# Kernel optimization log

Hardware: AMD Instinct MI355X
Metric: run time of the kernel (lower is better)

## Reference

```python
import jax, jax.numpy as jnp
import numpy as np

BATCH, BANDS, RESOLUTION = 8, 128, 64
N_FRAMES, N_SAMPLES = 128, 32768


def setup_inputs() -> dict:
    key = jax.random.key(0)
    k1, k2, k3 = jax.random.split(key, 3)
    x = jax.random.normal(k1, (BATCH, BANDS, RESOLUTION), dtype=jnp.float32)
    gumbel_noise = jax.random.gumbel(k2, (BATCH, BANDS, RESOLUTION), dtype=jnp.float32)
    # stand-in for morlet filter bank buffer (1, bands, n_samples)
    filter_bank = jax.random.normal(k3, (1, BANDS, N_SAMPLES), dtype=jnp.float32)
    # resonance buffer: linspace(0, 0.999, resolution) repeated over frames, cumprod over frames
    res = jnp.broadcast_to(jnp.linspace(0.0, 0.999, RESOLUTION, dtype=jnp.float32)[:, None],
                           (RESOLUTION, N_FRAMES))
    resonance = jnp.cumprod(res, axis=-1)  # (resolution, n_frames)
    return {"x": x, "gumbel_noise": gumbel_noise, "filter_bank": filter_bank, "resonance": resonance}


def _linear_interp_last(r, n_samples):
    # PyTorch F.interpolate(mode='linear', align_corners=False) on last axis
    n_in = r.shape[-1]
    scale = n_in / n_samples
    pos = (jnp.arange(n_samples, dtype=jnp.float32) + 0.5) * scale - 0.5
    pos = jnp.clip(pos, 0.0, n_in - 1)
    lo = jnp.floor(pos).astype(jnp.int32)
    hi = jnp.minimum(lo + 1, n_in - 1)
    w = (pos - lo.astype(jnp.float32)).astype(r.dtype)
    return r[..., lo] * (1.0 - w) + r[..., hi] * w


def reference(x, gumbel_noise, filter_bank, resonance):
    # gumbel_softmax with tau=1, hard=False: softmax(logits + gumbel_noise)
    g = jax.nn.softmax(x + gumbel_noise, axis=-1)              # (b, bands, resolution)
    r = jnp.einsum('bcr,rf->bcf', g, resonance)                # (b, bands, n_frames)
    up = _linear_interp_last(r, filter_bank.shape[-1])         # (b, bands, n_samples)
    out = jnp.mean(up * filter_bank, axis=1, keepdims=True)    # (b, 1, n_samples)
    return out
```

## Files before the change

kernel.cpp:

```cpp
#include <hip/hip_runtime.h>
#include <hip/hip_bf16.h>


#define BATCH 8
#define BANDS 128
#define RES 64
#define NF 128
#define NS 32768
#define SEG 512
#define NSEG (NS / SEG)
#define NBP 4
#define NTHR 512

__global__ __launch_bounds__(NTHR) void fused(const float* __restrict__ x,
                                              const float* __restrict__ gn,
                                              const float* __restrict__ fb,
                                              const float* __restrict__ res,
                                              float* __restrict__ out) {
    const int bi  = blockIdx.x;
    const int bp  = bi >> 6;
    const int seg = bi & 63;
    const int tid = threadIdx.x;

    __shared__ float resc[4][RES];
    __shared__ float r4[4][256];

    const int fbase = 2 * seg - 1;

    if (tid < 4 * RES) {
        const int rr = tid >> 2, j = tid & 3;
        const int f = min(max(fbase + j, 0), NF - 1);
        resc[j][rr] = res[rr * NF + f];
    }
    __syncthreads();

    const int e0 = (tid & 3) * 16;
    float4 cr[4][4];
    #pragma unroll
    for (int f = 0; f < 4; ++f)
        #pragma unroll
        for (int j = 0; j < 4; ++j)
            cr[f][j] = *(const float4*)&resc[f][e0 + 4 * j];

    const int q = tid >> 2;
    #pragma unroll
    for (int p = 0; p < 2; ++p) {
        const int row = p * 128 + q;
        const int bl  = row >> 7;
        const int c   = row & 127;
        const int bc  = (2 * bp + bl) * BANDS + c;

        const float4* __restrict__ xp = (const float4*)(x  + bc * RES + e0);
        const float4* __restrict__ gp = (const float4*)(gn + bc * RES + e0);

        float s = 0.f, d0 = 0.f, d1 = 0.f, d2 = 0.f, d3 = 0.f;
        #pragma unroll
        for (int j = 0; j < 4; ++j) {
            const float4 a = xp[j];
            const float4 b = gp[j];
            const float ex = __expf(a.x + b.x);
            const float ey = __expf(a.y + b.y);
            const float ez = __expf(a.z + b.z);
            const float ew = __expf(a.w + b.w);
            s += (ex + ey) + (ez + ew);
            d0 = fmaf(ex, cr[0][j].x, fmaf(ey, cr[0][j].y, fmaf(ez, cr[0][j].z, fmaf(ew, cr[0][j].w, d0))));
            d1 = fmaf(ex, cr[1][j].x, fmaf(ey, cr[1][j].y, fmaf(ez, cr[1][j].z, fmaf(ew, cr[1][j].w, d1))));
            d2 = fmaf(ex, cr[2][j].x, fmaf(ey, cr[2][j].y, fmaf(ez, cr[2][j].z, fmaf(ew, cr[2][j].w, d2))));
            d3 = fmaf(ex, cr[3][j].x, fmaf(ey, cr[3][j].y, fmaf(ez, cr[3][j].z, fmaf(ew, cr[3][j].w, d3))));
        }
        s  += __shfl_xor(s, 1);  s  += __shfl_xor(s, 2);
        d0 += __shfl_xor(d0, 1); d0 += __shfl_xor(d0, 2);
        d1 += __shfl_xor(d1, 1); d1 += __shfl_xor(d1, 2);
        d2 += __shfl_xor(d2, 1); d2 += __shfl_xor(d2, 2);
        d3 += __shfl_xor(d3, 1); d3 += __shfl_xor(d3, 2);

        if ((tid & 3) == 0) {
            const float inv = 1.0f / s;
            r4[0][row] = d0 * inv;
            r4[1][row] = d1 * inv;
            r4[2][row] = d2 * inv;
            r4[3][row] = d3 * inv;
        }
    }
    __syncthreads();

    const int bl = tid >> 8;
    const int d  = tid & 255;
    const int s0 = seg * SEG + 2 * d;

    float p0 = ((float)s0 + 0.5f) * (1.0f / 256.0f) - 0.5f;
    float p1 = ((float)s0 + 1.5f) * (1.0f / 256.0f) - 0.5f;
    p0 = fminf(fmaxf(p0, 0.0f), (float)(NF - 1));
    p1 = fminf(fmaxf(p1, 0.0f), (float)(NF - 1));
    const int lo = (int)floorf(p0);
    const int il = lo - fbase;
    const float w0 = p0 - (float)lo;
    const float w1 = p1 - (float)lo;

    const float* __restrict__ rl = &r4[il][bl * BANDS];
    const float* __restrict__ rh = &r4[il + 1][bl * BANDS];

    float acc0 = 0.f, acc1 = 0.f;
    #pragma unroll 8
    for (int cc = 0; cc < BANDS / 4; ++cc) {
        const float4 rl4 = *(const float4*)&rl[4 * cc];
        const float4 rh4 = *(const float4*)&rh[4 * cc];
        const int band0 = 4 * cc;

        const float2 f0 = *(const float2*)&fb[(band0 + 0) * NS + s0];
        const float2 f1 = *(const float2*)&fb[(band0 + 1) * NS + s0];
        const float2 f2 = *(const float2*)&fb[(band0 + 2) * NS + s0];
        const float2 f3 = *(const float2*)&fb[(band0 + 3) * NS + s0];

        const float dx = rh4.x - rl4.x, dy = rh4.y - rl4.y;
        const float dz = rh4.z - rl4.z, dw = rh4.w - rl4.w;

        acc0 = fmaf(f0.x, fmaf(w0, dx, rl4.x), acc0);
        acc1 = fmaf(f0.y, fmaf(w1, dx, rl4.x), acc1);
        acc0 = fmaf(f1.x, fmaf(w0, dy, rl4.y), acc0);
        acc1 = fmaf(f1.y, fmaf(w1, dy, rl4.y), acc1);
        acc0 = fmaf(f2.x, fmaf(w0, dz, rl4.z), acc0);
        acc1 = fmaf(f2.y, fmaf(w1, dz, rl4.z), acc1);
        acc0 = fmaf(f3.x, fmaf(w0, dw, rl4.w), acc0);
        acc1 = fmaf(f3.y, fmaf(w1, dw, rl4.w), acc1);
    }

    float2 o;
    o.x = acc0 * (1.0f / (float)BANDS);
    o.y = acc1 * (1.0f / (float)BANDS);
    *(float2*)&out[(2 * bp + bl) * NS + s0] = o;
}

extern "C" void kernel_launch(void* const* d_in, const int* in_sizes, int n_in,
                              void* d_out, int out_size, void* d_ws, size_t ws_size,
                              hipStream_t stream) {
    const float* x   = (const float*)d_in[0];
    const float* gn  = (const float*)d_in[1];
    const float* fb  = (const float*)d_in[2];
    const float* res = (const float*)d_in[3];
    float* out = (float*)d_out;

    fused<<<NBP * NSEG, NTHR, 0, stream>>>(x, gn, fb, res, out);
}
```

Baseline: 16.54 us.

## Split band reduction across waves and reuse filter loads for both batches

The second phase is restructured so each wave handles a quarter of the bands for a 256-sample half, with each thread covering 4 samples via float4 filter-bank loads. Each filter load now serves both batch rows in the block, so global filter traffic per block is halved. Partial sums go to a new shared buffer and are reduced across the four band groups after a barrier. This adds shared memory, an extra barrier and more registers per thread.

```diff
diff --git a/kernel.cpp b/kernel.cpp
--- a/kernel.cpp
+++ b/kernel.cpp
@@ -17,13 +17,16 @@
                                               const float* __restrict__ fb,
                                               const float* __restrict__ res,
                                               float* __restrict__ out) {
-    const int bi  = blockIdx.x;
-    const int bp  = bi >> 6;
-    const int seg = bi & 63;
-    const int tid = threadIdx.x;
+    const int bi   = blockIdx.x;
+    const int bp   = bi >> 6;
+    const int seg  = bi & 63;
+    const int tid  = threadIdx.x;
+    const int lane = tid & 63;
+    const int wv   = tid >> 6;
 
     __shared__ float resc[4][RES];
     __shared__ float r4[4][256];
+    __shared__ float part[4][2][SEG];
 
     const int fbase = 2 * seg - 1;
 
@@ -84,51 +87,102 @@
     }
     __syncthreads();
 
-    const int bl = tid >> 8;
-    const int d  = tid & 255;
-    const int s0 = seg * SEG + 2 * d;
+    const int bg  = wv >> 1;
+    const int sh  = wv & 1;
+    const int sl0 = sh * 256 + (lane << 2);
+    const int s0  = seg * SEG + sl0;
 
-    float p0 = ((float)s0 + 0.5f) * (1.0f / 256.0f) - 0.5f;
-    float p1 = ((float)s0 + 1.5f) * (1.0f / 256.0f) - 0.5f;
-    p0 = fminf(fmaxf(p0, 0.0f), (float)(NF - 1));
-    p1 = fminf(fmaxf(p1, 0.0f), (float)(NF - 1));
-    const int lo = (int)floorf(p0);
-    const int il = lo - fbase;
-    const float w0 = p0 - (float)lo;
-    const float w1 = p1 - (float)lo;
-
-    const float* __restrict__ rl = &r4[il][bl * BANDS];
-    const float* __restrict__ rh = &r4[il + 1][bl * BANDS];
-
-    float acc0 = 0.f, acc1 = 0.f;
-    #pragma unroll 8
-    for (int cc = 0; cc < BANDS / 4; ++cc) {
-        const float4 rl4 = *(const float4*)&rl[4 * cc];
-        const float4 rh4 = *(const float4*)&rh[4 * cc];
-        const int band0 = 4 * cc;
-
-        const float2 f0 = *(const float2*)&fb[(band0 + 0) * NS + s0];
-        const float2 f1 = *(const float2*)&fb[(band0 + 1) * NS + s0];
-        const float2 f2 = *(const float2*)&fb[(band0 + 2) * NS + s0];
-        const float2 f3 = *(const float2*)&fb[(band0 + 3) * NS + s0];
-
-        const float dx = rh4.x - rl4.x, dy = rh4.y - rl4.y;
-        const float dz = rh4.z - rl4.z, dw = rh4.w - rl4.w;
-
-        acc0 = fmaf(f0.x, fmaf(w0, dx, rl4.x), acc0);
-        acc1 = fmaf(f0.y, fmaf(w1, dx, rl4.x), acc1);
-        acc0 = fmaf(f1.x, fmaf(w0, dy, rl4.y), acc0);
-        acc1 = fmaf(f1.y, fmaf(w1, dy, rl4.y), acc1);
-        acc0 = fmaf(f2.x, fmaf(w0, dz, rl4.z), acc0);
-        acc1 = fmaf(f2.y, fmaf(w1, dz, rl4.z), acc1);
-        acc0 = fmaf(f3.x, fmaf(w0, dw, rl4.w), acc0);
-        acc1 = fmaf(f3.y, fmaf(w1, dw, rl4.w), acc1);
+    float w0, w1, w2, w3;
+    int il;
+    {
+        float pv[4];
+        #pragma unroll
+        for (int i = 0; i < 4; ++i) {
+            float p = ((float)(s0 + i) + 0.5f) * (1.0f / 256.0f) - 0.5f;
+            pv[i] = fminf(fmaxf(p, 0.0f), (float)(NF - 1));
+        }
+        const int lo = (int)floorf(pv[0]);
+        il = lo - fbase;
+        w0 = pv[0] - (float)lo; w1 = pv[1] - (float)lo;
+        w2 = pv[2] - (float)lo; w3 = pv[3] - (float)lo;
     }
 
+    const float* __restrict__ rlp = &r4[il][0];
+    const float* __restrict__ rhp = &r4[il + 1][0];
+    const int c0 = bg * 32;
+
+    float4 acc0 = {0.f, 0.f, 0.f, 0.f};
+    float4 acc1 = {0.f, 0.f, 0.f, 0.f};
+
+    #pragma unroll
+    for (int g = 0; g < 8; ++g) {
+        const int cb = c0 + g * 4;
+        const float4 f0 = *(const float4*)&fb[(cb + 0) * NS + s0];
+        const float4 f1 = *(const float4*)&fb[(cb + 1) * NS + s0];
+        const float4 f2 = *(const float4*)&fb[(cb + 2) * NS + s0];
+        const float4 f3 = *(const float4*)&fb[(cb + 3) * NS + s0];
+
+        {
+            const float4 rl4 = *(const float4*)&rlp[cb];
+            const float4 rh4 = *(const float4*)&rhp[cb];
+            const float dx = rh4.x - rl4.x, dy = rh4.y - rl4.y;
+            const float dz = rh4.z - rl4.z, dw = rh4.w - rl4.w;
+            acc0.x = fmaf(f0.x, fmaf(w0, dx, rl4.x), acc0.x);
+            acc0.y = fmaf(f0.y, fmaf(w1, dx, rl4.x), acc0.y);
+            acc0.z = fmaf(f0.z, fmaf(w2, dx, rl4.x), acc0.z);
+            acc0.w = fmaf(f0.w, fmaf(w3, dx, rl4.x), acc0.w);
+            acc0.x = fmaf(f1.x, fmaf(w0, dy, rl4.y), acc0.x);
+            acc0.y = fmaf(f1.y, fmaf(w1, dy, rl4.y), acc0.y);
+            acc0.z = fmaf(f1.z, fmaf(w2, dy, rl4.y), acc0.z);
+            acc0.w = fmaf(f1.w, fmaf(w3, dy, rl4.y), acc0.w);
+            acc0.x = fmaf(f2.x, fmaf(w0, dz, rl4.z), acc0.x);
+            acc0.y = fmaf(f2.y, fmaf(w1, dz, rl4.z), acc0.y);
+            acc0.z = fmaf(f2.z, fmaf(w2, dz, rl4.z), acc0.z);
+            acc0.w = fmaf(f2.w, fmaf(w3, dz, rl4.z), acc0.w);
+            acc0.x = fmaf(f3.x, fmaf(w0, dw, rl4.w), acc0.x);
+            acc0.y = fmaf(f3.y, fmaf(w1, dw, rl4.w), acc0.y);
+            acc0.z = fmaf(f3.z, fmaf(w2, dw, rl4.w), acc0.z);
+            acc0.w = fmaf(f3.w, fmaf(w3, dw, rl4.w), acc0.w);
+        }
+        {
+            const float4 rl4 = *(const float4*)&rlp[128 + cb];
+            const float4 rh4 = *(const float4*)&rhp[128 + cb];
+            const float dx = rh4.x - rl4.x, dy = rh4.y - rl4.y;
+            const float dz = rh4.z - rl4.z, dw = rh4.w - rl4.w;
+            acc1.x = fmaf(f0.x, fmaf(w0, dx, rl4.x), acc1.x);
+            acc1.y = fmaf(f0.y, fmaf(w1, dx, rl4.x), acc1.y);
+            acc1.z = fmaf(f0.z, fmaf(w2, dx, rl4.x), acc1.z);
+            acc1.w = fmaf(f0.w, fmaf(w3, dx, rl4.x), acc1.w);
+            acc1.x = fmaf(f1.x, fmaf(w0, dy, rl4.y), acc1.x);
+            acc1.y = fmaf(f1.y, fmaf(w1, dy, rl4.y), acc1.y);
+            acc1.z = fmaf(f1.z, fmaf(w2, dy, rl4.y), acc1.z);
+            acc1.w = fmaf(f1.w, fmaf(w3, dy, rl4.y), acc1.w);
+            acc1.x = fmaf(f2.x, fmaf(w0, dz, rl4.z), acc1.x);
+            acc1.y = fmaf(f2.y, fmaf(w1, dz, rl4.z), acc1.y);
+            acc1.z = fmaf(f2.z, fmaf(w2, dz, rl4.z), acc1.z);
+            acc1.w = fmaf(f2.w, fmaf(w3, dz, rl4.z), acc1.w);
+            acc1.x = fmaf(f3.x, fmaf(w0, dw, rl4.w), acc1.x);
+            acc1.y = fmaf(f3.y, fmaf(w1, dw, rl4.w), acc1.y);
+            acc1.z = fmaf(f3.z, fmaf(w2, dw, rl4.w), acc1.z);
+            acc1.w = fmaf(f3.w, fmaf(w3, dw, rl4.w), acc1.w);
+        }
+    }
+
+    *(float4*)&part[bg][0][sl0] = acc0;
+    *(float4*)&part[bg][1][sl0] = acc1;
+    __syncthreads();
+
+    const int bl2 = tid >> 8;
+    const int sp  = tid & 255;
+    const int ss  = sp * 2;
+    const float2 v0 = *(const float2*)&part[0][bl2][ss];
+    const float2 v1 = *(const float2*)&part[1][bl2][ss];
+    const float2 v2 = *(const float2*)&part[2][bl2][ss];
+    const float2 v3 = *(const float2*)&part[3][bl2][ss];
     float2 o;
-    o.x = acc0 * (1.0f / (float)BANDS);
-    o.y = acc1 * (1.0f / (float)BANDS);
-    *(float2*)&out[(2 * bp + bl) * NS + s0] = o;
+    o.x = ((v0.x + v1.x) + (v2.x + v3.x)) * (1.0f / (float)BANDS);
+    o.y = ((v0.y + v1.y) + (v2.y + v3.y)) * (1.0f / (float)BANDS);
+    *(float2*)&out[(2 * bp + bl2) * NS + seg * SEG + ss] = o;
 }
 
 extern "C" void kernel_launch(void* const* d_in, const int* in_sizes, int n_in,
```

New measurement: 14.89 us. -10.0%, faster.

## Halve segment size and reuse filter-bank loads across two batches per thread

Applied to the files above, without the earlier changes.

Segments shrink from 512 to 256 samples and blocks from 512 to 256 threads, so twice as many blocks run and each needs only 3 resonance frames instead of 4. In the interpolation phase only 128 threads work, and each handles both batches of its pair, so every filter-bank float2 load feeds both outputs instead of being loaded by two separate threads. The interpolation weight is applied once after the band reduction, using separate lo and hi accumulators instead of per-band blends. The trade-off is that half the threads sit idle in the second phase, each active thread does more FMAs, and the per-block softmax/resonance prologue is repeated across twice as many blocks.

```diff
diff --git a/kernel.cpp b/kernel.cpp
--- a/kernel.cpp
+++ b/kernel.cpp
@@ -7,10 +7,10 @@
 #define RES 64
 #define NF 128
 #define NS 32768
-#define SEG 512
+#define SEG 256
 #define NSEG (NS / SEG)
 #define NBP 4
-#define NTHR 512
+#define NTHR 256
 
 __global__ __launch_bounds__(NTHR) void fused(const float* __restrict__ x,
                                               const float* __restrict__ gn,
@@ -18,34 +18,34 @@
                                               const float* __restrict__ res,
                                               float* __restrict__ out) {
     const int bi  = blockIdx.x;
-    const int bp  = bi >> 6;
-    const int seg = bi & 63;
+    const int bp  = bi >> 7;
+    const int seg = bi & 127;
     const int tid = threadIdx.x;
 
-    __shared__ float resc[4][RES];
-    __shared__ float r4[4][256];
+    __shared__ float resc[3][RES];
+    __shared__ float r4[3][256];
 
-    const int fbase = 2 * seg - 1;
+    const int fbase = seg - 1;
 
-    if (tid < 4 * RES) {
-        const int rr = tid >> 2, j = tid & 3;
+    if (tid < 3 * RES) {
+        const int j = tid >> 6, rr = tid & 63;
         const int f = min(max(fbase + j, 0), NF - 1);
         resc[j][rr] = res[rr * NF + f];
     }
     __syncthreads();
 
     const int e0 = (tid & 3) * 16;
-    float4 cr[4][4];
+    float4 cr[3][4];
     #pragma unroll
-    for (int f = 0; f < 4; ++f)
+    for (int f = 0; f < 3; ++f)
         #pragma unroll
         for (int j = 0; j < 4; ++j)
             cr[f][j] = *(const float4*)&resc[f][e0 + 4 * j];
 
     const int q = tid >> 2;
     #pragma unroll
-    for (int p = 0; p < 2; ++p) {
-        const int row = p * 128 + q;
+    for (int p = 0; p < 4; ++p) {
+        const int row = p * 64 + q;
         const int bl  = row >> 7;
         const int c   = row & 127;
         const int bc  = (2 * bp + bl) * BANDS + c;
@@ -53,7 +53,7 @@
         const float4* __restrict__ xp = (const float4*)(x  + bc * RES + e0);
         const float4* __restrict__ gp = (const float4*)(gn + bc * RES + e0);
 
-        float s = 0.f, d0 = 0.f, d1 = 0.f, d2 = 0.f, d3 = 0.f;
+        float s = 0.f, d0 = 0.f, d1 = 0.f, d2 = 0.f;
         #pragma unroll
         for (int j = 0; j < 4; ++j) {
             const float4 a = xp[j];
@@ -66,26 +66,24 @@
             d0 = fmaf(ex, cr[0][j].x, fmaf(ey, cr[0][j].y, fmaf(ez, cr[0][j].z, fmaf(ew, cr[0][j].w, d0))));
             d1 = fmaf(ex, cr[1][j].x, fmaf(ey, cr[1][j].y, fmaf(ez, cr[1][j].z, fmaf(ew, cr[1][j].w, d1))));
             d2 = fmaf(ex, cr[2][j].x, fmaf(ey, cr[2][j].y, fmaf(ez, cr[2][j].z, fmaf(ew, cr[2][j].w, d2))));
-            d3 = fmaf(ex, cr[3][j].x, fmaf(ey, cr[3][j].y, fmaf(ez, cr[3][j].z, fmaf(ew, cr[3][j].w, d3))));
         }
         s  += __shfl_xor(s, 1);  s  += __shfl_xor(s, 2);
         d0 += __shfl_xor(d0, 1); d0 += __shfl_xor(d0, 2);
         d1 += __shfl_xor(d1, 1); d1 += __shfl_xor(d1, 2);
         d2 += __shfl_xor(d2, 1); d2 += __shfl_xor(d2, 2);
-        d3 += __shfl_xor(d3, 1); d3 += __shfl_xor(d3, 2);
 
         if ((tid & 3) == 0) {
             const float inv = 1.0f / s;
             r4[0][row] = d0 * inv;
             r4[1][row] = d1 * inv;
             r4[2][row] = d2 * inv;
-            r4[3][row] = d3 * inv;
         }
     }
     __syncthreads();
 
-    const int bl = tid >> 8;
-    const int d  = tid & 255;
+    if (tid >= 128) return;
+
+    const int d  = tid;
     const int s0 = seg * SEG + 2 * d;
 
     float p0 = ((float)s0 + 0.5f) * (1.0f / 256.0f) - 0.5f;
@@ -97,14 +95,18 @@
     const float w0 = p0 - (float)lo;
     const float w1 = p1 - (float)lo;
 
-    const float* __restrict__ rl = &r4[il][bl * BANDS];
-    const float* __restrict__ rh = &r4[il + 1][bl * BANDS];
+    const float* __restrict__ rlp = &r4[il][0];
+    const float* __restrict__ rhp = &r4[il + 1][0];
 
-    float acc0 = 0.f, acc1 = 0.f;
+    float2 lo0 = {0.f, 0.f}, hi0 = {0.f, 0.f};
+    float2 lo1 = {0.f, 0.f}, hi1 = {0.f, 0.f};
+
     #pragma unroll 8
     for (int cc = 0; cc < BANDS / 4; ++cc) {
-        const float4 rl4 = *(const float4*)&rl[4 * cc];
-        const float4 rh4 = *(const float4*)&rh[4 * cc];
+        const float4 a0 = *(const float4*)&rlp[4 * cc];
+        const float4 b0 = *(const float4*)&rhp[4 * cc];
+        const float4 a1 = *(const float4*)&rlp[128 + 4 * cc];
+        const float4 b1 = *(const float4*)&rhp[128 + 4 * cc];
         const int band0 = 4 * cc;
 
         const float2 f0 = *(const float2*)&fb[(band0 + 0) * NS + s0];
@@ -112,23 +114,35 @@
         const float2 f2 = *(const float2*)&fb[(band0 + 2) * NS + s0];
         const float2 f3 = *(const float2*)&fb[(band0 + 3) * NS + s0];
 
-        const float dx = rh4.x - rl4.x, dy = rh4.y - rl4.y;
-        const float dz = rh4.z - rl4.z, dw = rh4.w - rl4.w;
+        lo0.x = fmaf(f0.x, a0.x, lo0.x); lo0.y = fmaf(f0.y, a0.x, lo0.y);
+        hi0.x = fmaf(f0.x, b0.x, hi0.x); hi0.y = fmaf(f0.y, b0.x, hi0.y);
+        lo1.x = fmaf(f0.x, a1.x, lo1.x); lo1.y = fmaf(f0.y, a1.x, lo1.y);
+        hi1.x = fmaf(f0.x, b1.x, hi1.x); hi1.y = fmaf(f0.y, b1.x, hi1.y);
 
-        acc0 = fmaf(f0.x, fmaf(w0, dx, rl4.x), acc0);
-        acc1 = fmaf(f0.y, fmaf(w1, dx, rl4.x), acc1);
-        acc0 = fmaf(f1.x, fmaf(w0, dy, rl4.y), acc0);
-        acc1 = fmaf(f1.y, fmaf(w1, dy, rl4.y), acc1);
-        acc0 = fmaf(f2.x, fmaf(w0, dz, rl4.z), acc0);
-        acc1 = fmaf(f2.y, fmaf(w1, dz, rl4.z), acc1);
-        acc0 = fmaf(f3.x, fmaf(w0, dw, rl4.w), acc0);
-        acc1 = fmaf(f3.y, fmaf(w1, dw, rl4.w), acc1);
+        lo0.x = fmaf(f1.x, a0.y, lo0.x); lo0.y = fmaf(f1.y, a0.y, lo0.y);
+        hi0.x = fmaf(f1.x, b0.y, hi0.x); hi0.y = fmaf(f1.y, b0.y, hi0.y);
+        lo1.x = fmaf(f1.x, a1.y, lo1.x); lo1.y = fmaf(f1.y, a1.y, lo1.y);
+        hi1.x = fmaf(f1.x, b1.y, hi1.x); hi1.y = fmaf(f1.y, b1.y, hi1.y);
+
+        lo0.x = fmaf(f2.x, a0.z, lo0.x); lo0.y = fmaf(f2.y, a0.z, lo0.y);
+        hi0.x = fmaf(f2.x, b0.z, hi0.x); hi0.y = fmaf(f2.y, b0.z, hi0.y);
+        lo1.x = fmaf(f2.x, a1.z, lo1.x); lo1.y = fmaf(f2.y, a1.z, lo1.y);
+        hi1.x = fmaf(f2.x, b1.z, hi1.x); hi1.y = fmaf(f2.y, b1.z, hi1.y);
+
+        lo0.x = fmaf(f3.x, a0.w, lo0.x); lo0.y = fmaf(f3.y, a0.w, lo0.y);
+        hi0.x = fmaf(f3.x, b0.w, hi0.x); hi0.y = fmaf(f3.y, b0.w, hi0.y);
+        lo1.x = fmaf(f3.x, a1.w, lo1.x); lo1.y = fmaf(f3.y, a1.w, lo1.y);
+        hi1.x = fmaf(f3.x, b1.w, hi1.x); hi1.y = fmaf(f3.y, b1.w, hi1.y);
     }
 
-    float2 o;
-    o.x = acc0 * (1.0f / (float)BANDS);
-    o.y = acc1 * (1.0f / (float)BANDS);
-    *(float2*)&out[(2 * bp + bl) * NS + s0] = o;
+    const float sc = 1.0f / (float)BANDS;
+    float2 o0, o1;
+    o0.x = fmaf(w0, hi0.x - lo0.x, lo0.x) * sc;
+    o0.y = fmaf(w1, hi0.y - lo0.y, lo0.y) * sc;
+    o1.x = fmaf(w0, hi1.x - lo1.x, lo1.x) * sc;
+    o1.y = fmaf(w1, hi1.y - lo1.y, lo1.y) * sc;
+    *(float2*)&out[(2 * bp + 0) * NS + s0] = o0;
+    *(float2*)&out[(2 * bp + 1) * NS + s0] = o1;
 }
 
 extern "C" void kernel_launch(void* const* d_in, const int* in_sizes, int n_in,
```

Result: no change. 16.28 us (-1.6%).
